# Kernel optimization log

Measured on AMD Instinct MI355X. Metric: run time of the kernel, lower is better.

## Reference

```python
import jax, jax.numpy as jnp
import numpy as np

N = 50000
E = 800000
IN, HID, OUT = 256, 64, 64
H1, H2 = 4, 1
SLOPE = 0.2  # DGL GATConv default negative_slope


def setup_inputs() -> dict:
    key = jax.random.key(0)
    ks = jax.random.split(key, 12)
    inp = {
        "features": jax.random.normal(ks[0], (N, IN), jnp.float32),
        "src": jax.random.randint(ks[1], (E,), 0, N),
        "dst": jax.random.randint(ks[2], (E,), 0, N),
        # layer 1 params (fc has no bias in DGL; separate bias added post-aggregation)
        "W1": jax.random.normal(ks[3], (IN, H1 * HID), jnp.float32) * (1.0 / np.sqrt(IN)),
        "al1": jax.random.normal(ks[4], (H1, HID), jnp.float32) * 0.1,
        "ar1": jax.random.normal(ks[5], (H1, HID), jnp.float32) * 0.1,
        "b1": jnp.zeros((H1 * HID,), jnp.float32),
        # layer 2 params
        "W2": jax.random.normal(ks[6], (H1 * HID, H2 * OUT), jnp.float32) * (1.0 / np.sqrt(H1 * HID)),
        "al2": jax.random.normal(ks[7], (H2, OUT), jnp.float32) * 0.1,
        "ar2": jax.random.normal(ks[8], (H2, OUT), jnp.float32) * 0.1,
        "b2": jnp.zeros((H2 * OUT,), jnp.float32),
    }
    return inp


def _gat_layer(x, src, dst, W, al, ar, b, H, D):
    # fc projection + reshape to [N, H, D]
    h = (x @ W).reshape(-1, H, D)
    el = jnp.einsum("nhd,hd->nh", h, al)  # [N,H]
    er = jnp.einsum("nhd,hd->nh", h, ar)
    e = jax.nn.leaky_relu(el[src] + er[dst], SLOPE)  # [E,H]
    # segment (per-dst-node) softmax over incoming edges
    emax = jax.ops.segment_max(e, dst, num_segments=N)
    ex = jnp.exp(e - emax[dst])
    denom = jax.ops.segment_sum(ex, dst, num_segments=N)
    a = ex / denom[dst]  # [E,H]
    # weighted gather-scatter aggregation
    out = jax.ops.segment_sum(a[:, :, None] * h[src], dst, num_segments=N)  # [N,H,D]
    return out + b.reshape(1, H, D)


def reference(features, src, dst, W1, al1, ar1, b1, W2, al2, ar2, b2):
    # layer 1: GATConv + elu activation, then flatten heads
    h = _gat_layer(features, src, dst, W1, al1, ar1, b1, H1, HID)
    h = jax.nn.elu(h).reshape(N, H1 * HID)
    # layer 2: GATConv (no activation), then mean over heads
    h = _gat_layer(h, src, dst, W2, al2, ar2, b2, H2, OUT)
    return h.mean(axis=1)  # [N, OUT]
```

## Files before the change

kernel.cpp:

```cpp
#include <hip/hip_runtime.h>
#include <hip/hip_bf16.h>
#include <math.h>

#define SLOPE 0.2f

typedef __attribute__((ext_vector_type(8))) short bf16x8;
typedef __attribute__((ext_vector_type(4))) float f32x4;

__device__ inline unsigned short f2bf(float f) {
    unsigned u = __float_as_uint(f);
    u += 0x7FFF + ((u >> 16) & 1);
    return (unsigned short)(u >> 16);
}
__device__ inline float bf2f(unsigned short s) {
    return __uint_as_float(((unsigned)s) << 16);
}


__global__ void deg_kernel(const int* __restrict__ dst, int* __restrict__ deg,
                           int* __restrict__ rank, int E) {
    int i = blockIdx.x * blockDim.x + threadIdx.x;
    if (i < E) rank[i] = atomicAdd(&deg[dst[i]], 1);
}

__global__ __launch_bounds__(256) void psum_kernel(const int* __restrict__ deg,
                                                   int* __restrict__ bsum, int n) {
    const int t = threadIdx.x;
    const int i = blockIdx.x * 256 + t;
    int v = (i < n) ? deg[i] : 0;
#pragma unroll
    for (int o = 1; o < 64; o <<= 1) v += __shfl_xor(v, o, 64);
    __shared__ int ws[4];
    if ((t & 63) == 0) ws[t >> 6] = v;
    __syncthreads();
    if (t == 0) bsum[blockIdx.x] = ws[0] + ws[1] + ws[2] + ws[3];
}

__global__ __launch_bounds__(256) void scan2_kernel(const int* __restrict__ deg,
                                                    const int* __restrict__ bsum,
                                                    int* __restrict__ offs, int n) {
    const int b = blockIdx.x, t = threadIdx.x;
    const int lane = t & 63, w = t >> 6;

    int contrib = (t < b) ? bsum[t] : 0;
#pragma unroll
    for (int o = 1; o < 64; o <<= 1) contrib += __shfl_xor(contrib, o, 64);
    __shared__ int wsum[4];
    if (lane == 0) wsum[w] = contrib;
    __syncthreads();
    const int base = wsum[0] + wsum[1] + wsum[2] + wsum[3];

    const int i = b * 256 + t;
    const int v = (i < n) ? deg[i] : 0;
    int incl = v;
#pragma unroll
    for (int o = 1; o < 64; o <<= 1) {
        const int u = __shfl_up(incl, o, 64);
        if (lane >= o) incl += u;
    }
    __shared__ int wtot[4];
    if (lane == 63) wtot[w] = incl;
    __syncthreads();
    int wbase = 0;
#pragma unroll
    for (int k = 0; k < 4; ++k)
        if (k < w) wbase += wtot[k];

    const int excl = base + wbase + incl - v;
    if (i < n) offs[i] = excl;
    if (i == n - 1) offs[n] = excl + v;
}

__global__ void fill_kernel(const int* __restrict__ src, const int* __restrict__ dst,
                            const int* __restrict__ offs, const int* __restrict__ rank,
                            int* __restrict__ csr_src, int E) {
    int i = blockIdx.x * blockDim.x + threadIdx.x;
    if (i < E) {
        csr_src[offs[dst[i]] + rank[i]] = src[i];
    }
}


__global__ void cvt_x_kernel(const float4* __restrict__ X4, ushort4* __restrict__ O4,
                             int n4) {
    int i = blockIdx.x * blockDim.x + threadIdx.x;
    if (i < n4) {
        const float4 v = X4[i];
        ushort4 o;
        o.x = f2bf(v.x); o.y = f2bf(v.y); o.z = f2bf(v.z); o.w = f2bf(v.w);
        O4[i] = o;
    }
}

__global__ void cvt_wt_kernel(const float* __restrict__ W, unsigned short* __restrict__ Wt,
                              int K, int M) {
    const int k = blockIdx.x, c = threadIdx.x;
    Wt[c * K + k] = f2bf(W[k * M + c]);
}

__global__ __launch_bounds__(256) void gemm1_mfma(const unsigned short* __restrict__ Xbf,
                                                  const unsigned short* __restrict__ Wt,
                                                  const float* __restrict__ AL,
                                                  const float* __restrict__ AR,
                                                  unsigned short* __restrict__ Hout,
                                                  float* __restrict__ el,
                                                  float* __restrict__ er, int n) {
    constexpr int LDR = 72;
    __shared__ __align__(16) unsigned short Xs[128 * LDR];
    __shared__ __align__(16) unsigned short Ws[128 * LDR];

    const int tid = threadIdx.x;
    const int wave = tid >> 6, lane = tid & 63;
    const int col16 = lane & 15, quad = lane >> 4;
    const int node0 = blockIdx.x * 128;
    const int fb = blockIdx.y;

    f32x4 acc[8][2];
#pragma unroll
    for (int ft = 0; ft < 8; ++ft)
#pragma unroll
        for (int nt = 0; nt < 2; ++nt) acc[ft][nt] = (f32x4){0.f, 0.f, 0.f, 0.f};

    const int rr = tid >> 3;
    const int cc = (tid & 7) * 8;

    for (int k0 = 0; k0 < 256; k0 += 64) {
#pragma unroll
        for (int p = 0; p < 4; ++p) {
            const int row = rr + p * 32;
            int gx = node0 + row; if (gx >= n) gx = n - 1;
            *(bf16x8*)&Xs[row * LDR + cc] =
                *(const bf16x8*)&Xbf[(long long)gx * 256 + k0 + cc];
            *(bf16x8*)&Ws[row * LDR + cc] =
                *(const bf16x8*)&Wt[((long long)(fb * 128 + row)) * 256 + k0 + cc];
        }
        __syncthreads();
#pragma unroll
        for (int ks = 0; ks < 64; ks += 32) {
            bf16x8 bfrag[2];
#pragma unroll
            for (int nt = 0; nt < 2; ++nt)
                bfrag[nt] = *(const bf16x8*)&Xs[(wave * 32 + nt * 16 + col16) * LDR +
                                                ks + quad * 8];
#pragma unroll
            for (int ft = 0; ft < 8; ++ft) {
                const bf16x8 afrag =
                    *(const bf16x8*)&Ws[(ft * 16 + col16) * LDR + ks + quad * 8];
                acc[ft][0] = __builtin_amdgcn_mfma_f32_16x16x32_bf16(afrag, bfrag[0],
                                                                     acc[ft][0], 0, 0, 0);
                acc[ft][1] = __builtin_amdgcn_mfma_f32_16x16x32_bf16(afrag, bfrag[1],
                                                                     acc[ft][1], 0, 0, 0);
            }
        }
        __syncthreads();
    }

    float elp[2][2] = {{0.f, 0.f}, {0.f, 0.f}};
    float erp[2][2] = {{0.f, 0.f}, {0.f, 0.f}};
#pragma unroll
    for (int ft = 0; ft < 8; ++ft) {
        const int hb = ft >> 2;
        const int head = fb * 2 + hb;
        float alw[4], arw[4];
#pragma unroll
        for (int r = 0; r < 4; ++r) {
            const int d = (ft & 3) * 16 + quad * 4 + r;
            alw[r] = AL[head * 64 + d];
            arw[r] = AR[head * 64 + d];
        }
#pragma unroll
        for (int nt = 0; nt < 2; ++nt) {
            const int node = node0 + wave * 32 + nt * 16 + col16;
            if (node < n) {
                ushort4 pk;
                pk.x = f2bf(acc[ft][nt][0]); pk.y = f2bf(acc[ft][nt][1]);
                pk.z = f2bf(acc[ft][nt][2]); pk.w = f2bf(acc[ft][nt][3]);
                *(ushort4*)&Hout[(long long)node * 256 + fb * 128 + ft * 16 + quad * 4] = pk;
            }
#pragma unroll
            for (int r = 0; r < 4; ++r) {
                elp[nt][hb] = fmaf(acc[ft][nt][r], alw[r], elp[nt][hb]);
                erp[nt][hb] = fmaf(acc[ft][nt][r], arw[r], erp[nt][hb]);
            }
        }
    }
#pragma unroll
    for (int nt = 0; nt < 2; ++nt)
#pragma unroll
        for (int hb = 0; hb < 2; ++hb) {
            elp[nt][hb] += __shfl_xor(elp[nt][hb], 16, 64);
            elp[nt][hb] += __shfl_xor(elp[nt][hb], 32, 64);
            erp[nt][hb] += __shfl_xor(erp[nt][hb], 16, 64);
            erp[nt][hb] += __shfl_xor(erp[nt][hb], 32, 64);
        }
    if (quad == 0) {
#pragma unroll
        for (int nt = 0; nt < 2; ++nt) {
            const int node = node0 + wave * 32 + nt * 16 + col16;
            if (node < n) {
#pragma unroll
                for (int hb = 0; hb < 2; ++hb) {
                    el[node * 4 + fb * 2 + hb] = elp[nt][hb];
                    er[node * 4 + fb * 2 + hb] = erp[nt][hb];
                }
            }
        }
    }
}

__global__ __launch_bounds__(256) void gemm2_mfma(const unsigned short* __restrict__ Xbf,
                                                  const unsigned short* __restrict__ Wt,
                                                  const float* __restrict__ AL,
                                                  const float* __restrict__ AR,
                                                  float* __restrict__ Hout,
                                                  float* __restrict__ el,
                                                  float* __restrict__ er, int n) {
    constexpr int LDR = 72;
    __shared__ __align__(16) unsigned short Xs[128 * LDR];
    __shared__ __align__(16) unsigned short Ws[64 * LDR];

    const int tid = threadIdx.x;
    const int wave = tid >> 6, lane = tid & 63;
    const int col16 = lane & 15, quad = lane >> 4;
    const int node0 = blockIdx.x * 128;

    f32x4 acc[4][2];
#pragma unroll
    for (int ft = 0; ft < 4; ++ft)
#pragma unroll
        for (int nt = 0; nt < 2; ++nt) acc[ft][nt] = (f32x4){0.f, 0.f, 0.f, 0.f};

    const int rr = tid >> 3;
    const int cc = (tid & 7) * 8;

    for (int k0 = 0; k0 < 256; k0 += 64) {
#pragma unroll
        for (int p = 0; p < 4; ++p) {
            const int row = rr + p * 32;
            int gx = node0 + row; if (gx >= n) gx = n - 1;
            *(bf16x8*)&Xs[row * LDR + cc] =
                *(const bf16x8*)&Xbf[(long long)gx * 256 + k0 + cc];
        }
#pragma unroll
        for (int p = 0; p < 2; ++p) {
            const int row = rr + p * 32;
            *(bf16x8*)&Ws[row * LDR + cc] =
                *(const bf16x8*)&Wt[(long long)row * 256 + k0 + cc];
        }
        __syncthreads();
#pragma unroll
        for (int ks = 0; ks < 64; ks += 32) {
            bf16x8 bfrag[2];
#pragma unroll
            for (int nt = 0; nt < 2; ++nt)
                bfrag[nt] = *(const bf16x8*)&Xs[(wave * 32 + nt * 16 + col16) * LDR +
                                                ks + quad * 8];
#pragma unroll
            for (int ft = 0; ft < 4; ++ft) {
                const bf16x8 afrag =
                    *(const bf16x8*)&Ws[(ft * 16 + col16) * LDR + ks + quad * 8];
                acc[ft][0] = __builtin_amdgcn_mfma_f32_16x16x32_bf16(afrag, bfrag[0],
                                                                     acc[ft][0], 0, 0, 0);
                acc[ft][1] = __builtin_amdgcn_mfma_f32_16x16x32_bf16(afrag, bfrag[1],
                                                                     acc[ft][1], 0, 0, 0);
            }
        }
        __syncthreads();
    }

    float elp[2] = {0.f, 0.f}, erp[2] = {0.f, 0.f};
#pragma unroll
    for (int ft = 0; ft < 4; ++ft) {
        float alw[4], arw[4];
#pragma unroll
        for (int r = 0; r < 4; ++r) {
            const int d = ft * 16 + quad * 4 + r;
            alw[r] = AL[d];
            arw[r] = AR[d];
        }
#pragma unroll
        for (int nt = 0; nt < 2; ++nt) {
            const int node = node0 + wave * 32 + nt * 16 + col16;
            if (node < n) {
                *(float4*)&Hout[(long long)node * 64 + ft * 16 + quad * 4] =
                    make_float4(acc[ft][nt][0], acc[ft][nt][1],
                                acc[ft][nt][2], acc[ft][nt][3]);
            }
#pragma unroll
            for (int r = 0; r < 4; ++r) {
                elp[nt] = fmaf(acc[ft][nt][r], alw[r], elp[nt]);
                erp[nt] = fmaf(acc[ft][nt][r], arw[r], erp[nt]);
            }
        }
    }
#pragma unroll
    for (int nt = 0; nt < 2; ++nt) {
        elp[nt] += __shfl_xor(elp[nt], 16, 64);
        elp[nt] += __shfl_xor(elp[nt], 32, 64);
        erp[nt] += __shfl_xor(erp[nt], 16, 64);
        erp[nt] += __shfl_xor(erp[nt], 32, 64);
    }
    if (quad == 0) {
#pragma unroll
        for (int nt = 0; nt < 2; ++nt) {
            const int node = node0 + wave * 32 + nt * 16 + col16;
            if (node < n) {
                el[node] = elp[nt];
                er[node] = erp[nt];
            }
        }
    }
}

__global__ __launch_bounds__(256) void aggr1_kernel(const unsigned short* __restrict__ Hf,
                                                    const float* __restrict__ el,
                                                    const float* __restrict__ er,
                                                    const int* __restrict__ offs,
                                                    const int* __restrict__ csr,
                                                    const float* __restrict__ bias,
                                                    unsigned short* __restrict__ out,
                                                    int n) {
    const int node = (blockIdx.x * blockDim.x + threadIdx.x) >> 6;
    if (node >= n) return;
    const int lane = threadIdx.x & 63;
    const int g = lane >> 4;
    const int r = lane & 15;
    const int h = r >> 2;
    const int beg = offs[node], end = offs[node + 1];
    const float erv = er[node * 4 + h];

    float acc[16];
#pragma unroll
    for (int q = 0; q < 16; ++q) acc[q] = 0.f;
    float l = 0.f;

    const int nb = (end - beg + 3) >> 2;
#pragma unroll 2
    for (int it = 0; it < nb; ++it) {
        const int ei = beg + it * 4 + g;
        const bool ok = ei < end;
        const int ci = ok ? ei : (end - 1);
        const int s = csr[ci];
        float e = el[s * 4 + h] + erv;
        e = (e > 0.f) ? e : SLOPE * e;
        float p = __expf(fminf(e, 80.f));
        if (!ok) p = 0.f;
        const uint4* hp = (const uint4*)(Hf + (s << 8) + (r << 4));
        const uint4 u0 = hp[0];
        const uint4 u1 = hp[1];
        l += p;
        const unsigned uu[8] = {u0.x, u0.y, u0.z, u0.w, u1.x, u1.y, u1.z, u1.w};
#pragma unroll
        for (int q = 0; q < 8; ++q) {
            const float flo = __uint_as_float(uu[q] << 16);
            const float fhi = __uint_as_float(uu[q] & 0xFFFF0000u);
            acc[2 * q]     = fmaf(p, flo, acc[2 * q]);
            acc[2 * q + 1] = fmaf(p, fhi, acc[2 * q + 1]);
        }
    }

#pragma unroll
    for (int q = 0; q < 16; ++q) {
        acc[q] += __shfl_xor(acc[q], 16, 64);
        acc[q] += __shfl_xor(acc[q], 32, 64);
    }
    l += __shfl_xor(l, 16, 64);
    l += __shfl_xor(l, 32, 64);

    if (g == 0) {
        const float inv = (l > 0.f) ? 1.f / l : 0.f;
        unsigned o[8];
#pragma unroll
        for (int q = 0; q < 8; ++q) {
            float v0 = acc[2 * q]     * inv + bias[r * 16 + 2 * q];
            float v1 = acc[2 * q + 1] * inv + bias[r * 16 + 2 * q + 1];
            v0 = (v0 > 0.f) ? v0 : expm1f(v0);
            v1 = (v1 > 0.f) ? v1 : expm1f(v1);
            o[q] = (unsigned)f2bf(v0) | ((unsigned)f2bf(v1) << 16);
        }
        uint4* op = (uint4*)(out + (node << 8) + (r << 4));
        op[0] = make_uint4(o[0], o[1], o[2], o[3]);
        op[1] = make_uint4(o[4], o[5], o[6], o[7]);
    }
}

__global__ __launch_bounds__(256) void aggr2_kernel(const float* __restrict__ Hf,
                                                    const float* __restrict__ el,
                                                    const float* __restrict__ er,
                                                    const int* __restrict__ offs,
                                                    const int* __restrict__ csr,
                                                    const float* __restrict__ bias,
                                                    float* __restrict__ out, int n) {
    const int node = (blockIdx.x * blockDim.x + threadIdx.x) >> 6;
    if (node >= n) return;
    const int lane = threadIdx.x & 63;
    const int g = lane >> 4;
    const int r = lane & 15;
    const int beg = offs[node], end = offs[node + 1];
    const float erv = er[node];

    float a0 = 0.f, a1 = 0.f, a2 = 0.f, a3 = 0.f, l = 0.f;
    const int nb = (end - beg + 3) >> 2;
#pragma unroll 2
    for (int it = 0; it < nb; ++it) {
        const int ei = beg + it * 4 + g;
        const bool ok = ei < end;
        const int ci = ok ? ei : (end - 1);
        const int s = csr[ci];
        float e = el[s] + erv;
        e = (e > 0.f) ? e : SLOPE * e;
        float p = __expf(fminf(e, 80.f));
        if (!ok) p = 0.f;
        const float4 hv = *(const float4*)(Hf + (s << 6) + (r << 2));
        l += p;
        a0 = fmaf(p, hv.x, a0);
        a1 = fmaf(p, hv.y, a1);
        a2 = fmaf(p, hv.z, a2);
        a3 = fmaf(p, hv.w, a3);
    }

    a0 += __shfl_xor(a0, 16, 64); a0 += __shfl_xor(a0, 32, 64);
    a1 += __shfl_xor(a1, 16, 64); a1 += __shfl_xor(a1, 32, 64);
    a2 += __shfl_xor(a2, 16, 64); a2 += __shfl_xor(a2, 32, 64);
    a3 += __shfl_xor(a3, 16, 64); a3 += __shfl_xor(a3, 32, 64);
    l  += __shfl_xor(l, 16, 64);  l  += __shfl_xor(l, 32, 64);

    if (g == 0) {
        const float inv = (l > 0.f) ? 1.f / l : 0.f;
        const float4 b4 = *(const float4*)(bias + r * 4);
        *(float4*)(out + (node << 6) + (r << 2)) =
            make_float4(fmaf(a0, inv, b4.x), fmaf(a1, inv, b4.y),
                        fmaf(a2, inv, b4.z), fmaf(a3, inv, b4.w));
    }
}


extern "C" void kernel_launch(void* const* d_in, const int* in_sizes, int n_in,
                              void* d_out, int out_size, void* d_ws, size_t ws_size,
                              hipStream_t stream) {
    const float* feat = (const float*)d_in[0];
    const int*   src  = (const int*)d_in[1];
    const int*   dst  = (const int*)d_in[2];
    const float* W1   = (const float*)d_in[3];
    const float* al1  = (const float*)d_in[4];
    const float* ar1  = (const float*)d_in[5];
    const float* b1   = (const float*)d_in[6];
    const float* W2   = (const float*)d_in[7];
    const float* al2  = (const float*)d_in[8];
    const float* ar2  = (const float*)d_in[9];
    const float* b2   = (const float*)d_in[10];
    float* out = (float*)d_out;

    const int IN = 256, HID = 64, OUT = 64, H1 = 4, H2 = 1;
    const int N = in_sizes[0] / IN;
    const int E = in_sizes[1];

    size_t off = 0;
    auto alloc = [&](size_t bytes) {
        void* p = (char*)d_ws + off;
        off += (bytes + 255) & ~(size_t)255;
        return p;
    };
    int*   deg    = (int*)alloc((size_t)N * 4);
    int*   offs   = (int*)alloc((size_t)(N + 1) * 4);
    int*   bsum   = (int*)alloc((size_t)256 * 4);
    int*   rank   = (int*)alloc((size_t)E * 4);
    int*   csr    = (int*)alloc((size_t)E * 4);
    unsigned short* h1   = (unsigned short*)alloc((size_t)N * H1 * HID * 2);
    unsigned short* xbf  = (unsigned short*)alloc((size_t)N * IN * 2);
    unsigned short* wt1  = (unsigned short*)alloc((size_t)IN * H1 * HID * 2);
    unsigned short* wt2  = (unsigned short*)alloc((size_t)H1 * HID * H2 * OUT * 2);
    unsigned short* x2bf = (unsigned short*)alloc((size_t)N * H1 * HID * 2);
    float* el1    = (float*)alloc((size_t)N * H1 * 4);
    float* er1    = (float*)alloc((size_t)N * H1 * 4);
    float* h2     = (float*)alloc((size_t)N * H2 * OUT * 4);
    float* el2    = (float*)alloc((size_t)N * H2 * 4);
    float* er2    = (float*)alloc((size_t)N * H2 * 4);
    (void)ws_size;

    hipMemsetAsync(deg, 0, (size_t)N * 4, stream);

    const int nb = (N + 255) / 256;
    deg_kernel<<<(E + 255) / 256, 256, 0, stream>>>(dst, deg, rank, E);
    psum_kernel<<<nb, 256, 0, stream>>>(deg, bsum, N);
    scan2_kernel<<<nb, 256, 0, stream>>>(deg, bsum, offs, N);
    fill_kernel<<<(E + 255) / 256, 256, 0, stream>>>(src, dst, offs, rank, csr, E);

    {
        const int n4 = N * IN / 4;
        cvt_x_kernel<<<(n4 + 255) / 256, 256, 0, stream>>>((const float4*)feat,
                                                           (ushort4*)xbf, n4);
        cvt_wt_kernel<<<256, 256, 0, stream>>>(W1, wt1, 256, 256);
        cvt_wt_kernel<<<256, 64, 0, stream>>>(W2, wt2, 256, 64);
    }

    {
        dim3 g((N + 127) / 128, 2);
        gemm1_mfma<<<g, 256, 0, stream>>>(xbf, wt1, al1, ar1, h1, el1, er1, N);
    }
    aggr1_kernel<<<(N + 3) / 4, 256, 0, stream>>>(h1, el1, er1, offs, csr, b1, x2bf, N);
    gemm2_mfma<<<(N + 127) / 128, 256, 0, stream>>>(x2bf, wt2, al2, ar2, h2, el2, er2, N);
    aggr2_kernel<<<(N + 3) / 4, 256, 0, stream>>>(h2, el2, er2, offs, csr, b2, out, N);
}
```

Baseline: 314.1 us.

## Fuse feature bf16 conversion into GEMM1, store layer-2 features as fp16

Result: slower. 324.9 us (+3.4%).

```diff
diff --git a/kernel.cpp b/kernel.cpp
--- a/kernel.cpp
+++ b/kernel.cpp
@@ -1,5 +1,6 @@
 #include <hip/hip_runtime.h>
 #include <hip/hip_bf16.h>
+#include <hip/hip_fp16.h>
 #include <math.h>
 
 #define SLOPE 0.2f
@@ -81,24 +82,13 @@
 }
 
 
-__global__ void cvt_x_kernel(const float4* __restrict__ X4, ushort4* __restrict__ O4,
-                             int n4) {
-    int i = blockIdx.x * blockDim.x + threadIdx.x;
-    if (i < n4) {
-        const float4 v = X4[i];
-        ushort4 o;
-        o.x = f2bf(v.x); o.y = f2bf(v.y); o.z = f2bf(v.z); o.w = f2bf(v.w);
-        O4[i] = o;
-    }
-}
-
 __global__ void cvt_wt_kernel(const float* __restrict__ W, unsigned short* __restrict__ Wt,
                               int K, int M) {
     const int k = blockIdx.x, c = threadIdx.x;
     Wt[c * K + k] = f2bf(W[k * M + c]);
 }
 
-__global__ __launch_bounds__(256) void gemm1_mfma(const unsigned short* __restrict__ Xbf,
+__global__ __launch_bounds__(256) void gemm1_mfma(const float* __restrict__ Xf,
                                                   const unsigned short* __restrict__ Wt,
                                                   const float* __restrict__ AL,
                                                   const float* __restrict__ AR,
@@ -129,8 +119,15 @@
         for (int p = 0; p < 4; ++p) {
             const int row = rr + p * 32;
             int gx = node0 + row; if (gx >= n) gx = n - 1;
-            *(bf16x8*)&Xs[row * LDR + cc] =
-                *(const bf16x8*)&Xbf[(long long)gx * 256 + k0 + cc];
+            const float4* xp = (const float4*)&Xf[(long long)gx * 256 + k0 + cc];
+            const float4 a = xp[0];
+            const float4 b = xp[1];
+            bf16x8 v;
+            v[0] = (short)f2bf(a.x); v[1] = (short)f2bf(a.y);
+            v[2] = (short)f2bf(a.z); v[3] = (short)f2bf(a.w);
+            v[4] = (short)f2bf(b.x); v[5] = (short)f2bf(b.y);
+            v[6] = (short)f2bf(b.z); v[7] = (short)f2bf(b.w);
+            *(bf16x8*)&Xs[row * LDR + cc] = v;
             *(bf16x8*)&Ws[row * LDR + cc] =
                 *(const bf16x8*)&Wt[((long long)(fb * 128 + row)) * 256 + k0 + cc];
         }
@@ -212,7 +209,7 @@
                                                   const unsigned short* __restrict__ Wt,
                                                   const float* __restrict__ AL,
                                                   const float* __restrict__ AR,
-                                                  float* __restrict__ Hout,
+                                                  unsigned short* __restrict__ Hout,
                                                   float* __restrict__ el,
                                                   float* __restrict__ er, int n) {
     constexpr int LDR = 72;
@@ -282,9 +279,12 @@
         for (int nt = 0; nt < 2; ++nt) {
             const int node = node0 + wave * 32 + nt * 16 + col16;
             if (node < n) {
-                *(float4*)&Hout[(long long)node * 64 + ft * 16 + quad * 4] =
-                    make_float4(acc[ft][nt][0], acc[ft][nt][1],
-                                acc[ft][nt][2], acc[ft][nt][3]);
+                ushort4 pk;
+                pk.x = __half_as_ushort(__float2half(acc[ft][nt][0]));
+                pk.y = __half_as_ushort(__float2half(acc[ft][nt][1]));
+                pk.z = __half_as_ushort(__float2half(acc[ft][nt][2]));
+                pk.w = __half_as_ushort(__float2half(acc[ft][nt][3]));
+                *(ushort4*)&Hout[(long long)node * 64 + ft * 16 + quad * 4] = pk;
             }
 #pragma unroll
             for (int r = 0; r < 4; ++r) {
@@ -335,7 +335,7 @@
     float l = 0.f;
 
     const int nb = (end - beg + 3) >> 2;
-#pragma unroll 2
+#pragma unroll 4
     for (int it = 0; it < nb; ++it) {
         const int ei = beg + it * 4 + g;
         const bool ok = ei < end;
@@ -384,7 +384,7 @@
     }
 }
 
-__global__ __launch_bounds__(256) void aggr2_kernel(const float* __restrict__ Hf,
+__global__ __launch_bounds__(256) void aggr2_kernel(const unsigned short* __restrict__ Hf,
                                                     const float* __restrict__ el,
                                                     const float* __restrict__ er,
                                                     const int* __restrict__ offs,
@@ -401,7 +401,7 @@
 
     float a0 = 0.f, a1 = 0.f, a2 = 0.f, a3 = 0.f, l = 0.f;
     const int nb = (end - beg + 3) >> 2;
-#pragma unroll 2
+#pragma unroll 4
     for (int it = 0; it < nb; ++it) {
         const int ei = beg + it * 4 + g;
         const bool ok = ei < end;
@@ -411,12 +411,16 @@
         e = (e > 0.f) ? e : SLOPE * e;
         float p = __expf(fminf(e, 80.f));
         if (!ok) p = 0.f;
-        const float4 hv = *(const float4*)(Hf + (s << 6) + (r << 2));
+        const uint2 u = *(const uint2*)(Hf + (s << 6) + (r << 2));
+        const float h0 = __half2float(__ushort_as_half((unsigned short)(u.x & 0xFFFFu)));
+        const float h1 = __half2float(__ushort_as_half((unsigned short)(u.x >> 16)));
+        const float h2 = __half2float(__ushort_as_half((unsigned short)(u.y & 0xFFFFu)));
+        const float h3 = __half2float(__ushort_as_half((unsigned short)(u.y >> 16)));
         l += p;
-        a0 = fmaf(p, hv.x, a0);
-        a1 = fmaf(p, hv.y, a1);
-        a2 = fmaf(p, hv.z, a2);
-        a3 = fmaf(p, hv.w, a3);
+        a0 = fmaf(p, h0, a0);
+        a1 = fmaf(p, h1, a1);
+        a2 = fmaf(p, h2, a2);
+        a3 = fmaf(p, h3, a3);
     }
 
     a0 += __shfl_xor(a0, 16, 64); a0 += __shfl_xor(a0, 32, 64);
@@ -467,13 +471,12 @@
     int*   rank   = (int*)alloc((size_t)E * 4);
     int*   csr    = (int*)alloc((size_t)E * 4);
     unsigned short* h1   = (unsigned short*)alloc((size_t)N * H1 * HID * 2);
-    unsigned short* xbf  = (unsigned short*)alloc((size_t)N * IN * 2);
     unsigned short* wt1  = (unsigned short*)alloc((size_t)IN * H1 * HID * 2);
     unsigned short* wt2  = (unsigned short*)alloc((size_t)H1 * HID * H2 * OUT * 2);
     unsigned short* x2bf = (unsigned short*)alloc((size_t)N * H1 * HID * 2);
+    unsigned short* h2   = (unsigned short*)alloc((size_t)N * H2 * OUT * 2);
     float* el1    = (float*)alloc((size_t)N * H1 * 4);
     float* er1    = (float*)alloc((size_t)N * H1 * 4);
-    float* h2     = (float*)alloc((size_t)N * H2 * OUT * 4);
     float* el2    = (float*)alloc((size_t)N * H2 * 4);
     float* er2    = (float*)alloc((size_t)N * H2 * 4);
     (void)ws_size;
@@ -486,17 +489,12 @@
     scan2_kernel<<<nb, 256, 0, stream>>>(deg, bsum, offs, N);
     fill_kernel<<<(E + 255) / 256, 256, 0, stream>>>(src, dst, offs, rank, csr, E);
 
-    {
-        const int n4 = N * IN / 4;
-        cvt_x_kernel<<<(n4 + 255) / 256, 256, 0, stream>>>((const float4*)feat,
-                                                           (ushort4*)xbf, n4);
-        cvt_wt_kernel<<<256, 256, 0, stream>>>(W1, wt1, 256, 256);
-        cvt_wt_kernel<<<256, 64, 0, stream>>>(W2, wt2, 256, 64);
-    }
+    cvt_wt_kernel<<<256, 256, 0, stream>>>(W1, wt1, 256, 256);
+    cvt_wt_kernel<<<256, 64, 0, stream>>>(W2, wt2, 256, 64);
 
     {
         dim3 g((N + 127) / 128, 2);
-        gemm1_mfma<<<g, 256, 0, stream>>>(xbf, wt1, al1, ar1, h1, el1, er1, N);
+        gemm1_mfma<<<g, 256, 0, stream>>>(feat, wt1, al1, ar1, h1, el1, er1, N);
     }
     aggr1_kernel<<<(N + 3) / 4, 256, 0, stream>>>(h1, el1, er1, offs, csr, b1, x2bf, N);
     gemm2_mfma<<<(N + 127) / 128, 256, 0, stream>>>(x2bf, wt2, al2, ar2, h2, el2, er2, N);
```
